# Kernel tuning notes

Measured on AMD Instinct MI355X. Metric: run time of the kernel, lower is better.

The kernel has to match this reference:

```python
import jax, jax.numpy as jnp
import numpy as np

N = 8192
D_IN = 512
D_HID = 256
D_OUT = 128
NEG_SLOPE = 0.25
MASK_VAL = -1.0e12
EDGE_PROB = 0.004  # avg degree ~33


def _leaky(x):
    return jax.nn.leaky_relu(x, NEG_SLOPE)


def setup_inputs() -> dict:
    key = jax.random.key(0)
    ks = jax.random.split(key, 9)
    x = jax.random.normal(ks[0], (N, D_IN), jnp.float32)
    # sparse-ish normalized adjacency, stored dense (torch uses sparse mm / to_dense)
    vals = jax.random.uniform(ks[1], (N, N), jnp.float32)
    mask = jax.random.uniform(ks[2], (N, N)) < EDGE_PROB
    adj = jnp.where(mask, vals, 0.0).astype(jnp.float32)
    W1 = jax.random.normal(ks[3], (D_IN, D_HID), jnp.float32) * (2.0 / (D_IN + D_HID)) ** 0.5
    b1 = jnp.zeros((D_HID,), jnp.float32)
    W2 = jax.random.normal(ks[4], (D_HID, D_HID), jnp.float32) * (1.0 / D_HID) ** 0.5
    b2 = jnp.zeros((D_HID,), jnp.float32)
    Wg = jax.random.normal(ks[5], (D_HID, D_OUT), jnp.float32) * (2.0 / (D_HID + D_OUT)) ** 0.5
    a = jax.random.normal(ks[6], (2 * D_OUT, 1), jnp.float32) * 0.1
    return dict(x=x, adj=adj, W1=W1, b1=b1, W2=W2, b2=b2, Wg=Wg, a=a)


def reference(x, adj, W1, b1, W2, b2, Wg, a):
    # GCN layer 1: adj @ (x @ W1) + b1, leaky_relu (dropout p=0 / eval -> identity)
    x1 = _leaky(adj @ (x @ W1) + b1)
    # GCN layer 2
    x2 = _leaky(adj @ (x1 @ W2) + b2)
    # GAT layer: h = x2 @ Wg; e[i,j] = leaky_relu([h_i || h_j] @ a)
    # identical to leaky_relu((h@a1)_i + (h@a2)_j) without the O(N^2*2F) concat
    h = x2 @ Wg                              # [N, D_OUT]
    a1 = a[:D_OUT, 0]
    a2 = a[D_OUT:, 0]
    e = _leaky((h @ a1)[:, None] + (h @ a2)[None, :])  # [N, N]
    att = jnp.where(adj > 0, e, MASK_VAL)
    att = jax.nn.softmax(att, axis=1)
    h_prime = att @ h                        # [N, D_OUT] (concat=False -> no elu)
    out = _leaky(h_prime)
    mu = out[:, : D_OUT // 2]
    logvar = out[:, D_OUT // 2 :]
    return mu, logvar
```

## Files before the change

### kernel.cpp

```cpp
#include <hip/hip_runtime.h>

typedef unsigned short u16;
typedef u16 u16x4 __attribute__((ext_vector_type(4)));
typedef __bf16 bf16x8 __attribute__((ext_vector_type(8)));
typedef float f32x4 __attribute__((ext_vector_type(4)));

#define NROW 8192
#define CAP 128
#define D_IN 512
#define D_HID 256
#define D_OUT 128

__device__ __forceinline__ float leaky_f(float x) { return x > 0.f ? x : 0.25f * x; }

__device__ __forceinline__ u16 f2bf_rne(float f) {
  unsigned u = __float_as_uint(f);
  u += 0x7fffu + ((u >> 16) & 1u);
  return (u16)(u >> 16);
}
__device__ __forceinline__ void split_bf16(float f, u16& hi, u16& lo) {
  hi = f2bf_rne(f);
  float fh = __uint_as_float(((unsigned)hi) << 16);
  lo = f2bf_rne(f - fh);
}

__global__ __launch_bounds__(256) void k_csr_packw(const float* __restrict__ adj,
    int* __restrict__ cnt, int* __restrict__ cols, float* __restrict__ vals,
    const float* __restrict__ W1, u16* __restrict__ B1,
    const float* __restrict__ W2, u16* __restrict__ B2,
    const float* __restrict__ Wg, u16* __restrict__ B3) {
  int b = blockIdx.x;
  if (b < NROW) {
    int i = b;
    __shared__ int c;
    if (threadIdx.x == 0) c = 0;
    __syncthreads();
    const float4* row = (const float4*)(adj + (size_t)i * NROW);
    for (int j4 = threadIdx.x; j4 < NROW / 4; j4 += 256) {
      float4 v = row[j4];
      int base = j4 * 4;
      if (v.x > 0.f) { int s = atomicAdd(&c, 1); if (s < CAP) { cols[i*CAP+s] = base;   vals[i*CAP+s] = v.x; } }
      if (v.y > 0.f) { int s = atomicAdd(&c, 1); if (s < CAP) { cols[i*CAP+s] = base+1; vals[i*CAP+s] = v.y; } }
      if (v.z > 0.f) { int s = atomicAdd(&c, 1); if (s < CAP) { cols[i*CAP+s] = base+2; vals[i*CAP+s] = v.z; } }
      if (v.w > 0.f) { int s = atomicAdd(&c, 1); if (s < CAP) { cols[i*CAP+s] = base+3; vals[i*CAP+s] = v.w; } }
    }
    __syncthreads();
    if (threadIdx.x == 0) cnt[i] = (c < CAP) ? c : CAP;
    return;
  }
  const float* W; u16* Bt; int K, Nc, id;
  int pb = b - NROW;
  if (pb < 512)      { W = W1; Bt = B1; K = D_IN;  Nc = D_HID; id = pb * 256 + threadIdx.x; }
  else if (pb < 768) { W = W2; Bt = B2; K = D_HID; Nc = D_HID; id = (pb - 512) * 256 + threadIdx.x; }
  else               { W = Wg; Bt = B3; K = D_HID; Nc = D_OUT; id = (pb - 768) * 256 + threadIdx.x; }
  int n = id % Nc, k = id / Nc;
  float f = W[id];
  u16 hi, lo; split_bf16(f, hi, lo);
  size_t ro = (size_t)n * 2 * K;
  Bt[ro + k] = hi; Bt[ro + K + k] = lo;
}

__global__ __launch_bounds__(256) void k_gemm_x(const float* __restrict__ X, const u16* __restrict__ Bt,
    float* __restrict__ C, int N, int K) {
  __shared__ u16 Ah[64 * 40], Al[64 * 40];
  __shared__ u16 Bh[64 * 40], Bl[64 * 40];
  int tid = threadIdx.x;
  int bm = blockIdx.y * 64, bn = blockIdx.x * 64;
  int wave = tid >> 6, lane = tid & 63, l15 = lane & 15, quad = lane >> 4;
  f32x4 acc[4] = {};
  int ar = tid >> 2, aj = (tid & 3) << 3;
  const float* Xrow = X + (size_t)(bm + ar) * K + aj;
  const u16* Brow = Bt + (size_t)(bn + ar) * (2 * K) + aj;
  for (int k0 = 0; k0 < K; k0 += 32) {
    alignas(16) u16 hh[8], ll[8];
    float xv[8];
    *(float4*)(xv)     = *(const float4*)(Xrow + k0);
    *(float4*)(xv + 4) = *(const float4*)(Xrow + k0 + 4);
#pragma unroll
    for (int e = 0; e < 8; ++e) split_bf16(xv[e], hh[e], ll[e]);
    *(uint4*)(&Ah[ar * 40 + aj]) = *(const uint4*)hh;
    *(uint4*)(&Al[ar * 40 + aj]) = *(const uint4*)ll;
    *(uint4*)(&Bh[ar * 40 + aj]) = *(const uint4*)(Brow + k0);
    *(uint4*)(&Bl[ar * 40 + aj]) = *(const uint4*)(Brow + K + k0);
    __syncthreads();
    bf16x8 afh = *(const bf16x8*)(&Ah[(wave * 16 + l15) * 40 + quad * 8]);
    bf16x8 afl = *(const bf16x8*)(&Al[(wave * 16 + l15) * 40 + quad * 8]);
#pragma unroll
    for (int c = 0; c < 4; ++c) {
      bf16x8 bfh = *(const bf16x8*)(&Bh[(c * 16 + l15) * 40 + quad * 8]);
      bf16x8 bfl = *(const bf16x8*)(&Bl[(c * 16 + l15) * 40 + quad * 8]);
      acc[c] = __builtin_amdgcn_mfma_f32_16x16x32_bf16(afh, bfh, acc[c], 0, 0, 0);
      acc[c] = __builtin_amdgcn_mfma_f32_16x16x32_bf16(afh, bfl, acc[c], 0, 0, 0);
      acc[c] = __builtin_amdgcn_mfma_f32_16x16x32_bf16(afl, bfh, acc[c], 0, 0, 0);
    }
    __syncthreads();
  }
#pragma unroll
  for (int c = 0; c < 4; ++c)
#pragma unroll
    for (int rg = 0; rg < 4; ++rg) {
      int rowi = bm + wave * 16 + quad * 4 + rg;
      int coli = bn + c * 16 + l15;
      C[(size_t)rowi * N + coli] = acc[c][rg];
    }
}

__global__ __launch_bounds__(256) void k_gemm(const u16* __restrict__ A, const u16* __restrict__ Bt,
    float* __restrict__ C, int N, int K) {
  __shared__ u16 Ah[64 * 40], Al[64 * 40];
  __shared__ u16 Bh[64 * 40], Bl[64 * 40];
  int tid = threadIdx.x;
  int bm = blockIdx.y * 64, bn = blockIdx.x * 64;
  int wave = tid >> 6, lane = tid & 63, l15 = lane & 15, quad = lane >> 4;
  f32x4 acc[4] = {};
  int ar = tid >> 2, aj = (tid & 3) << 3;
  const u16* Arow = A + (size_t)(bm + ar) * (2 * K) + aj;
  const u16* Brow = Bt + (size_t)(bn + ar) * (2 * K) + aj;
  for (int k0 = 0; k0 < K; k0 += 32) {
    *(uint4*)(&Ah[ar * 40 + aj]) = *(const uint4*)(Arow + k0);
    *(uint4*)(&Al[ar * 40 + aj]) = *(const uint4*)(Arow + K + k0);
    *(uint4*)(&Bh[ar * 40 + aj]) = *(const uint4*)(Brow + k0);
    *(uint4*)(&Bl[ar * 40 + aj]) = *(const uint4*)(Brow + K + k0);
    __syncthreads();
    bf16x8 afh = *(const bf16x8*)(&Ah[(wave * 16 + l15) * 40 + quad * 8]);
    bf16x8 afl = *(const bf16x8*)(&Al[(wave * 16 + l15) * 40 + quad * 8]);
#pragma unroll
    for (int c = 0; c < 4; ++c) {
      bf16x8 bfh = *(const bf16x8*)(&Bh[(c * 16 + l15) * 40 + quad * 8]);
      bf16x8 bfl = *(const bf16x8*)(&Bl[(c * 16 + l15) * 40 + quad * 8]);
      acc[c] = __builtin_amdgcn_mfma_f32_16x16x32_bf16(afh, bfh, acc[c], 0, 0, 0);
      acc[c] = __builtin_amdgcn_mfma_f32_16x16x32_bf16(afh, bfl, acc[c], 0, 0, 0);
      acc[c] = __builtin_amdgcn_mfma_f32_16x16x32_bf16(afl, bfh, acc[c], 0, 0, 0);
    }
    __syncthreads();
  }
#pragma unroll
  for (int c = 0; c < 4; ++c)
#pragma unroll
    for (int rg = 0; rg < 4; ++rg) {
      int rowi = bm + wave * 16 + quad * 4 + rg;
      int coli = bn + c * 16 + l15;
      C[(size_t)rowi * N + coli] = acc[c][rg];
    }
}

__global__ __launch_bounds__(256) void k_gemm3(const u16* __restrict__ A, const u16* __restrict__ Bt,
    float* __restrict__ C, int K,
    const float* __restrict__ aptr, float* __restrict__ s1, float* __restrict__ s2) {
  __shared__ u16 Ah[32 * 40], Al[32 * 40];
  __shared__ u16 Bh[128 * 40], Bl[128 * 40];
  __shared__ float sp1[2][32], sp2[2][32];
  int tid = threadIdx.x;
  int bm = blockIdx.y * 32;
  int wave = tid >> 6, lane = tid & 63, l15 = lane & 15, quad = lane >> 4;
  int rhalf = wave >> 1, chalf = wave & 1;
  f32x4 acc[4] = {};
  int t7 = tid & 127;
  int ar = t7 >> 2, aj = (t7 & 3) << 3;
  int br = tid >> 1, bj = (tid & 1) << 4;
  const u16* Arow = A + (size_t)(bm + ar) * (2 * K) + aj + (tid < 128 ? 0 : K);
  u16* Adst = (tid < 128 ? Ah : Al) + ar * 40 + aj;
  const u16* Brow = Bt + (size_t)br * (2 * K) + bj;
  for (int k0 = 0; k0 < K; k0 += 32) {
    *(uint4*)Adst = *(const uint4*)(Arow + k0);
#pragma unroll
    for (int jj = 0; jj < 2; ++jj) {
      *(uint4*)(&Bh[br * 40 + bj + jj * 8]) = *(const uint4*)(Brow + k0 + jj * 8);
      *(uint4*)(&Bl[br * 40 + bj + jj * 8]) = *(const uint4*)(Brow + K + k0 + jj * 8);
    }
    __syncthreads();
    bf16x8 afh = *(const bf16x8*)(&Ah[(rhalf * 16 + l15) * 40 + quad * 8]);
    bf16x8 afl = *(const bf16x8*)(&Al[(rhalf * 16 + l15) * 40 + quad * 8]);
#pragma unroll
    for (int c = 0; c < 4; ++c) {
      bf16x8 bfh = *(const bf16x8*)(&Bh[(chalf * 64 + c * 16 + l15) * 40 + quad * 8]);
      bf16x8 bfl = *(const bf16x8*)(&Bl[(chalf * 64 + c * 16 + l15) * 40 + quad * 8]);
      acc[c] = __builtin_amdgcn_mfma_f32_16x16x32_bf16(afh, bfh, acc[c], 0, 0, 0);
      acc[c] = __builtin_amdgcn_mfma_f32_16x16x32_bf16(afh, bfl, acc[c], 0, 0, 0);
      acc[c] = __builtin_amdgcn_mfma_f32_16x16x32_bf16(afl, bfh, acc[c], 0, 0, 0);
    }
    __syncthreads();
  }
#pragma unroll
  for (int c = 0; c < 4; ++c)
#pragma unroll
    for (int rg = 0; rg < 4; ++rg) {
      int rowi = bm + rhalf * 16 + quad * 4 + rg;
      int coli = chalf * 64 + c * 16 + l15;
      C[(size_t)rowi * 128 + coli] = acc[c][rg];
    }
  float a1v[4], a2v[4];
#pragma unroll
  for (int c = 0; c < 4; ++c) {
    a1v[c] = aptr[chalf * 64 + c * 16 + l15];
    a2v[c] = aptr[128 + chalf * 64 + c * 16 + l15];
  }
#pragma unroll
  for (int rg = 0; rg < 4; ++rg) {
    float p1 = 0.f, p2 = 0.f;
#pragma unroll
    for (int c = 0; c < 4; ++c) { p1 = fmaf(acc[c][rg], a1v[c], p1); p2 = fmaf(acc[c][rg], a2v[c], p2); }
#pragma unroll
    for (int m = 1; m < 16; m <<= 1) { p1 += __shfl_xor(p1, m); p2 += __shfl_xor(p2, m); }
    if (l15 == 0) {
      int rloc = rhalf * 16 + quad * 4 + rg;
      sp1[chalf][rloc] = p1; sp2[chalf][rloc] = p2;
    }
  }
  __syncthreads();
  if (tid < 32) {
    s1[bm + tid] = sp1[0][tid] + sp1[1][tid];
    s2[bm + tid] = sp2[0][tid] + sp2[1][tid];
  }
}

__global__ __launch_bounds__(256) void k_spmm_pack(const float* __restrict__ Hin,
    const float* __restrict__ bias, const int* __restrict__ cnt,
    const int* __restrict__ cols, const float* __restrict__ vals, u16* __restrict__ Ap) {
  int i = blockIdx.x, t = threadIdx.x;
  int t64 = t & 63, g = t >> 6;
  __shared__ int sc[CAP];
  __shared__ float sv[CAP];
  __shared__ float4 sacc[4][64];
  int n = cnt[i];
  if (t < n) { sc[t] = cols[i * CAP + t]; sv[t] = vals[i * CAP + t]; }
  __syncthreads();
  float4 acc = {0.f, 0.f, 0.f, 0.f};
  const float4* H4 = (const float4*)Hin;
  for (int k = g; k < n; k += 4) {
    float w = sv[k];
    float4 v = H4[(size_t)sc[k] * 64 + t64];
    acc.x = fmaf(w, v.x, acc.x); acc.y = fmaf(w, v.y, acc.y);
    acc.z = fmaf(w, v.z, acc.z); acc.w = fmaf(w, v.w, acc.w);
  }
  sacc[g][t64] = acc;
  __syncthreads();
  if (t < 64) {
    float4 a0 = sacc[0][t], a1 = sacc[1][t], a2 = sacc[2][t], a3 = sacc[3][t];
    float4 bv = ((const float4*)bias)[t];
    float r[4] = { leaky_f(a0.x + a1.x + a2.x + a3.x + bv.x),
                   leaky_f(a0.y + a1.y + a2.y + a3.y + bv.y),
                   leaky_f(a0.z + a1.z + a2.z + a3.z + bv.z),
                   leaky_f(a0.w + a1.w + a2.w + a3.w + bv.w) };
    u16x4 hi4, lo4;
#pragma unroll
    for (int e = 0; e < 4; ++e) { u16 hh, ll; split_bf16(r[e], hh, ll); hi4[e] = hh; lo4[e] = ll; }
    size_t ro = (size_t)i * 512;
    *(u16x4*)(Ap + ro + 4 * t) = hi4;
    *(u16x4*)(Ap + ro + 256 + 4 * t) = lo4;
  }
}

__global__ __launch_bounds__(128) void k_attn(const float* __restrict__ h,
    const float* __restrict__ s1, const float* __restrict__ s2,
    const int* __restrict__ cnt, const int* __restrict__ cols, float* __restrict__ out) {
  int i = blockIdx.x, t = threadIdx.x;
  int t32 = t & 31, g = t >> 5;
  __shared__ int sc[CAP];
  __shared__ float sw[CAP];
  __shared__ float sred[2];
  __shared__ float4 sacc[4][32];
  int n = cnt[i];
  float s1i = s1[i];
  if (t < n) { int c = cols[i * CAP + t]; sc[t] = c; sw[t] = leaky_f(s1i + s2[c]); }
  __syncthreads();
  if (t < 64) {
    float m = -1e30f;
    if (t < n) m = sw[t];
    if (t + 64 < n) m = fmaxf(m, sw[t + 64]);
    for (int o = 32; o > 0; o >>= 1) m = fmaxf(m, __shfl_down(m, o));
    if (t == 0) sred[0] = m;
  }
  __syncthreads();
  float mx = sred[0];
  if (t < n) sw[t] = expf(sw[t] - mx);
  __syncthreads();
  if (t < 64) {
    float s = 0.f;
    if (t < n) s = sw[t];
    if (t + 64 < n) s += sw[t + 64];
    for (int o = 32; o > 0; o >>= 1) s += __shfl_down(s, o);
    if (t == 0) sred[1] = s;
  }
  __syncthreads();
  float inv = (n > 0) ? 1.0f / sred[1] : 0.f;
  float4 acc = {0.f, 0.f, 0.f, 0.f};
  const float4* h4 = (const float4*)h;
  for (int k = g; k < n; k += 4) {
    float w = sw[k];
    float4 v = h4[(size_t)sc[k] * 32 + t32];
    acc.x = fmaf(w, v.x, acc.x); acc.y = fmaf(w, v.y, acc.y);
    acc.z = fmaf(w, v.z, acc.z); acc.w = fmaf(w, v.w, acc.w);
  }
  sacc[g][t32] = acc;
  __syncthreads();
  if (t < 32) {
    float4 a0 = sacc[0][t], a1 = sacc[1][t], a2 = sacc[2][t], a3 = sacc[3][t];
    float4 r;
    r.x = leaky_f((a0.x + a1.x + a2.x + a3.x) * inv);
    r.y = leaky_f((a0.y + a1.y + a2.y + a3.y) * inv);
    r.z = leaky_f((a0.z + a1.z + a2.z + a3.z) * inv);
    r.w = leaky_f((a0.w + a1.w + a2.w + a3.w) * inv);
    float4* o4 = (float4*)out;
    if (t < 16) o4[(size_t)i * 16 + t] = r;
    else        o4[(size_t)NROW * 16 + (size_t)i * 16 + (t - 16)] = r;
  }
}

extern "C" void kernel_launch(void* const* d_in, const int* in_sizes, int n_in,
                              void* d_out, int out_size, void* d_ws, size_t ws_size,
                              hipStream_t stream) {
  const float* x   = (const float*)d_in[0];
  const float* adj = (const float*)d_in[1];
  const float* W1  = (const float*)d_in[2];
  const float* b1  = (const float*)d_in[3];
  const float* W2  = (const float*)d_in[4];
  const float* b2  = (const float*)d_in[5];
  const float* Wg  = (const float*)d_in[6];
  const float* a   = (const float*)d_in[7];
  float* out = (float*)d_out;

  char* ws = (char*)d_ws;
  int*   row_cnt  = (int*)  (ws + 0);
  int*   row_cols = (int*)  (ws + 32768);
  float* row_vals = (float*)(ws + 4227072);
  u16*   B1t      = (u16*)  (ws + 8421376);
  u16*   B2t      = (u16*)  (ws + 8945664);
  u16*   B3t      = (u16*)  (ws + 9207808);
  float* s1       = (float*)(ws + 9338880);
  float* s2       = (float*)(ws + 9371648);
  float* h        = (float*)(ws + 9404416);
  float* H0T2     = (float*)(ws + 13598720);
  u16*   Apack    = (u16*)  (ws + 21987328);

  k_csr_packw<<<NROW + 896, 256, 0, stream>>>(adj, row_cnt, row_cols, row_vals,
                                              W1, B1t, W2, B2t, Wg, B3t);
  k_gemm_x<<<dim3(4, 128), 256, 0, stream>>>(x, B1t, H0T2, D_HID, D_IN);
  k_spmm_pack<<<NROW, 256, 0, stream>>>(H0T2, b1, row_cnt, row_cols, row_vals, Apack);
  k_gemm<<<dim3(4, 128), 256, 0, stream>>>(Apack, B2t, H0T2, D_HID, D_HID);
  k_spmm_pack<<<NROW, 256, 0, stream>>>(H0T2, b2, row_cnt, row_cols, row_vals, Apack);
  k_gemm3<<<dim3(1, 256), 256, 0, stream>>>(Apack, B3t, h, D_HID, a, s1, s2);
  k_attn<<<NROW, 128, 0, stream>>>(h, s1, s2, row_cnt, row_cols, out);
}
```

Measured before the change: 494.4 us.

## Fuse CSR build with first GEMM and store GAT features as bf16

Moves the CSR extraction of the dense adjacency out of the weight-packing kernel and into the first x@W1 GEMM launch, so the memory-bound adjacency scan runs alongside the MFMA GEMM blocks. Weight packing now runs as its own small kernel first. Separately, the GAT feature matrix h is written as bf16 instead of fp32, halving the bytes gathered in the attention aggregation. The bf16 storage of h lowers precision of the final output.

```diff
diff --git a/kernel.cpp b/kernel.cpp
--- a/kernel.cpp
+++ b/kernel.cpp
@@ -18,38 +18,19 @@
   u += 0x7fffu + ((u >> 16) & 1u);
   return (u16)(u >> 16);
 }
+__device__ __forceinline__ float bf2f(u16 v) { return __uint_as_float(((unsigned)v) << 16); }
 __device__ __forceinline__ void split_bf16(float f, u16& hi, u16& lo) {
   hi = f2bf_rne(f);
   float fh = __uint_as_float(((unsigned)hi) << 16);
   lo = f2bf_rne(f - fh);
 }
 
-__global__ __launch_bounds__(256) void k_csr_packw(const float* __restrict__ adj,
-    int* __restrict__ cnt, int* __restrict__ cols, float* __restrict__ vals,
+__global__ __launch_bounds__(256) void k_packw(
     const float* __restrict__ W1, u16* __restrict__ B1,
     const float* __restrict__ W2, u16* __restrict__ B2,
     const float* __restrict__ Wg, u16* __restrict__ B3) {
-  int b = blockIdx.x;
-  if (b < NROW) {
-    int i = b;
-    __shared__ int c;
-    if (threadIdx.x == 0) c = 0;
-    __syncthreads();
-    const float4* row = (const float4*)(adj + (size_t)i * NROW);
-    for (int j4 = threadIdx.x; j4 < NROW / 4; j4 += 256) {
-      float4 v = row[j4];
-      int base = j4 * 4;
-      if (v.x > 0.f) { int s = atomicAdd(&c, 1); if (s < CAP) { cols[i*CAP+s] = base;   vals[i*CAP+s] = v.x; } }
-      if (v.y > 0.f) { int s = atomicAdd(&c, 1); if (s < CAP) { cols[i*CAP+s] = base+1; vals[i*CAP+s] = v.y; } }
-      if (v.z > 0.f) { int s = atomicAdd(&c, 1); if (s < CAP) { cols[i*CAP+s] = base+2; vals[i*CAP+s] = v.z; } }
-      if (v.w > 0.f) { int s = atomicAdd(&c, 1); if (s < CAP) { cols[i*CAP+s] = base+3; vals[i*CAP+s] = v.w; } }
-    }
-    __syncthreads();
-    if (threadIdx.x == 0) cnt[i] = (c < CAP) ? c : CAP;
-    return;
-  }
   const float* W; u16* Bt; int K, Nc, id;
-  int pb = b - NROW;
+  int pb = blockIdx.x;
   if (pb < 512)      { W = W1; Bt = B1; K = D_IN;  Nc = D_HID; id = pb * 256 + threadIdx.x; }
   else if (pb < 768) { W = W2; Bt = B2; K = D_HID; Nc = D_HID; id = (pb - 512) * 256 + threadIdx.x; }
   else               { W = Wg; Bt = B3; K = D_HID; Nc = D_OUT; id = (pb - 768) * 256 + threadIdx.x; }
@@ -60,49 +41,70 @@
   Bt[ro + k] = hi; Bt[ro + K + k] = lo;
 }
 
-__global__ __launch_bounds__(256) void k_gemm_x(const float* __restrict__ X, const u16* __restrict__ Bt,
-    float* __restrict__ C, int N, int K) {
+__global__ __launch_bounds__(256) void k_csr_gemm1(const float* __restrict__ adj,
+    int* __restrict__ cnt, int* __restrict__ cols, float* __restrict__ vals,
+    const float* __restrict__ X, const u16* __restrict__ Bt, float* __restrict__ C) {
   __shared__ u16 Ah[64 * 40], Al[64 * 40];
   __shared__ u16 Bh[64 * 40], Bl[64 * 40];
+  __shared__ int csrc;
+  int b = blockIdx.x;
   int tid = threadIdx.x;
-  int bm = blockIdx.y * 64, bn = blockIdx.x * 64;
-  int wave = tid >> 6, lane = tid & 63, l15 = lane & 15, quad = lane >> 4;
-  f32x4 acc[4] = {};
-  int ar = tid >> 2, aj = (tid & 3) << 3;
-  const float* Xrow = X + (size_t)(bm + ar) * K + aj;
-  const u16* Brow = Bt + (size_t)(bn + ar) * (2 * K) + aj;
-  for (int k0 = 0; k0 < K; k0 += 32) {
-    alignas(16) u16 hh[8], ll[8];
-    float xv[8];
-    *(float4*)(xv)     = *(const float4*)(Xrow + k0);
-    *(float4*)(xv + 4) = *(const float4*)(Xrow + k0 + 4);
-#pragma unroll
-    for (int e = 0; e < 8; ++e) split_bf16(xv[e], hh[e], ll[e]);
-    *(uint4*)(&Ah[ar * 40 + aj]) = *(const uint4*)hh;
-    *(uint4*)(&Al[ar * 40 + aj]) = *(const uint4*)ll;
-    *(uint4*)(&Bh[ar * 40 + aj]) = *(const uint4*)(Brow + k0);
-    *(uint4*)(&Bl[ar * 40 + aj]) = *(const uint4*)(Brow + K + k0);
-    __syncthreads();
-    bf16x8 afh = *(const bf16x8*)(&Ah[(wave * 16 + l15) * 40 + quad * 8]);
-    bf16x8 afl = *(const bf16x8*)(&Al[(wave * 16 + l15) * 40 + quad * 8]);
-#pragma unroll
-    for (int c = 0; c < 4; ++c) {
-      bf16x8 bfh = *(const bf16x8*)(&Bh[(c * 16 + l15) * 40 + quad * 8]);
-      bf16x8 bfl = *(const bf16x8*)(&Bl[(c * 16 + l15) * 40 + quad * 8]);
-      acc[c] = __builtin_amdgcn_mfma_f32_16x16x32_bf16(afh, bfh, acc[c], 0, 0, 0);
-      acc[c] = __builtin_amdgcn_mfma_f32_16x16x32_bf16(afh, bfl, acc[c], 0, 0, 0);
-      acc[c] = __builtin_amdgcn_mfma_f32_16x16x32_bf16(afl, bfh, acc[c], 0, 0, 0);
-    }
-    __syncthreads();
-  }
-#pragma unroll
-  for (int c = 0; c < 4; ++c)
-#pragma unroll
-    for (int rg = 0; rg < 4; ++rg) {
-      int rowi = bm + wave * 16 + quad * 4 + rg;
-      int coli = bn + c * 16 + l15;
-      C[(size_t)rowi * N + coli] = acc[c][rg];
-    }
+  if (b < 512) {
+    const int N = D_HID, K = D_IN;
+    int bm = (b >> 2) * 64, bn = (b & 3) * 64;
+    int wave = tid >> 6, lane = tid & 63, l15 = lane & 15, quad = lane >> 4;
+    f32x4 acc[4] = {};
+    int ar = tid >> 2, aj = (tid & 3) << 3;
+    const float* Xrow = X + (size_t)(bm + ar) * K + aj;
+    const u16* Brow = Bt + (size_t)(bn + ar) * (2 * K) + aj;
+    for (int k0 = 0; k0 < K; k0 += 32) {
+      alignas(16) u16 hh[8], ll[8];
+      float xv[8];
+      *(float4*)(xv)     = *(const float4*)(Xrow + k0);
+      *(float4*)(xv + 4) = *(const float4*)(Xrow + k0 + 4);
+#pragma unroll
+      for (int e = 0; e < 8; ++e) split_bf16(xv[e], hh[e], ll[e]);
+      *(uint4*)(&Ah[ar * 40 + aj]) = *(const uint4*)hh;
+      *(uint4*)(&Al[ar * 40 + aj]) = *(const uint4*)ll;
+      *(uint4*)(&Bh[ar * 40 + aj]) = *(const uint4*)(Brow + k0);
+      *(uint4*)(&Bl[ar * 40 + aj]) = *(const uint4*)(Brow + K + k0);
+      __syncthreads();
+      bf16x8 afh = *(const bf16x8*)(&Ah[(wave * 16 + l15) * 40 + quad * 8]);
+      bf16x8 afl = *(const bf16x8*)(&Al[(wave * 16 + l15) * 40 + quad * 8]);
+#pragma unroll
+      for (int c = 0; c < 4; ++c) {
+        bf16x8 bfh = *(const bf16x8*)(&Bh[(c * 16 + l15) * 40 + quad * 8]);
+        bf16x8 bfl = *(const bf16x8*)(&Bl[(c * 16 + l15) * 40 + quad * 8]);
+        acc[c] = __builtin_amdgcn_mfma_f32_16x16x32_bf16(afh, bfh, acc[c], 0, 0, 0);
+        acc[c] = __builtin_amdgcn_mfma_f32_16x16x32_bf16(afh, bfl, acc[c], 0, 0, 0);
+        acc[c] = __builtin_amdgcn_mfma_f32_16x16x32_bf16(afl, bfh, acc[c], 0, 0, 0);
+      }
+      __syncthreads();
+    }
+#pragma unroll
+    for (int c = 0; c < 4; ++c)
+#pragma unroll
+      for (int rg = 0; rg < 4; ++rg) {
+        int rowi = bm + wave * 16 + quad * 4 + rg;
+        int coli = bn + c * 16 + l15;
+        C[(size_t)rowi * N + coli] = acc[c][rg];
+      }
+    return;
+  }
+  int i = b - 512;
+  if (tid == 0) csrc = 0;
+  __syncthreads();
+  const float4* row = (const float4*)(adj + (size_t)i * NROW);
+  for (int j4 = tid; j4 < NROW / 4; j4 += 256) {
+    float4 v = row[j4];
+    int base = j4 * 4;
+    if (v.x > 0.f) { int s = atomicAdd(&csrc, 1); if (s < CAP) { cols[i*CAP+s] = base;   vals[i*CAP+s] = v.x; } }
+    if (v.y > 0.f) { int s = atomicAdd(&csrc, 1); if (s < CAP) { cols[i*CAP+s] = base+1; vals[i*CAP+s] = v.y; } }
+    if (v.z > 0.f) { int s = atomicAdd(&csrc, 1); if (s < CAP) { cols[i*CAP+s] = base+2; vals[i*CAP+s] = v.z; } }
+    if (v.w > 0.f) { int s = atomicAdd(&csrc, 1); if (s < CAP) { cols[i*CAP+s] = base+3; vals[i*CAP+s] = v.w; } }
+  }
+  __syncthreads();
+  if (tid == 0) cnt[i] = (csrc < CAP) ? csrc : CAP;
 }
 
 __global__ __launch_bounds__(256) void k_gemm(const u16* __restrict__ A, const u16* __restrict__ Bt,
@@ -145,7 +147,7 @@
 }
 
 __global__ __launch_bounds__(256) void k_gemm3(const u16* __restrict__ A, const u16* __restrict__ Bt,
-    float* __restrict__ C, int K,
+    u16* __restrict__ Hb, int K,
     const float* __restrict__ aptr, float* __restrict__ s1, float* __restrict__ s2) {
   __shared__ u16 Ah[32 * 40], Al[32 * 40];
   __shared__ u16 Bh[128 * 40], Bl[128 * 40];
@@ -187,7 +189,7 @@
     for (int rg = 0; rg < 4; ++rg) {
       int rowi = bm + rhalf * 16 + quad * 4 + rg;
       int coli = chalf * 64 + c * 16 + l15;
-      C[(size_t)rowi * 128 + coli] = acc[c][rg];
+      Hb[(size_t)rowi * 128 + coli] = f2bf_rne(acc[c][rg]);
     }
   float a1v[4], a2v[4];
 #pragma unroll
@@ -251,7 +253,7 @@
   }
 }
 
-__global__ __launch_bounds__(128) void k_attn(const float* __restrict__ h,
+__global__ __launch_bounds__(128) void k_attn(const u16* __restrict__ Hb,
     const float* __restrict__ s1, const float* __restrict__ s2,
     const int* __restrict__ cnt, const int* __restrict__ cols, float* __restrict__ out) {
   int i = blockIdx.x, t = threadIdx.x;
@@ -285,12 +287,11 @@
   __syncthreads();
   float inv = (n > 0) ? 1.0f / sred[1] : 0.f;
   float4 acc = {0.f, 0.f, 0.f, 0.f};
-  const float4* h4 = (const float4*)h;
   for (int k = g; k < n; k += 4) {
     float w = sw[k];
-    float4 v = h4[(size_t)sc[k] * 32 + t32];
-    acc.x = fmaf(w, v.x, acc.x); acc.y = fmaf(w, v.y, acc.y);
-    acc.z = fmaf(w, v.z, acc.z); acc.w = fmaf(w, v.w, acc.w);
+    u16x4 v = *(const u16x4*)(Hb + (size_t)sc[k] * 128 + 4 * t32);
+    acc.x = fmaf(w, bf2f(v[0]), acc.x); acc.y = fmaf(w, bf2f(v[1]), acc.y);
+    acc.z = fmaf(w, bf2f(v[2]), acc.z); acc.w = fmaf(w, bf2f(v[3]), acc.w);
   }
   sacc[g][t32] = acc;
   __syncthreads();
@@ -329,16 +330,15 @@
   u16*   B3t      = (u16*)  (ws + 9207808);
   float* s1       = (float*)(ws + 9338880);
   float* s2       = (float*)(ws + 9371648);
-  float* h        = (float*)(ws + 9404416);
+  u16*   hbf      = (u16*)  (ws + 9404416);
   float* H0T2     = (float*)(ws + 13598720);
   u16*   Apack    = (u16*)  (ws + 21987328);
 
-  k_csr_packw<<<NROW + 896, 256, 0, stream>>>(adj, row_cnt, row_cols, row_vals,
-                                              W1, B1t, W2, B2t, Wg, B3t);
-  k_gemm_x<<<dim3(4, 128), 256, 0, stream>>>(x, B1t, H0T2, D_HID, D_IN);
+  k_packw<<<896, 256, 0, stream>>>(W1, B1t, W2, B2t, Wg, B3t);
+  k_csr_gemm1<<<512 + NROW, 256, 0, stream>>>(adj, row_cnt, row_cols, row_vals, x, B1t, H0T2);
   k_spmm_pack<<<NROW, 256, 0, stream>>>(H0T2, b1, row_cnt, row_cols, row_vals, Apack);
   k_gemm<<<dim3(4, 128), 256, 0, stream>>>(Apack, B2t, H0T2, D_HID, D_HID);
   k_spmm_pack<<<NROW, 256, 0, stream>>>(H0T2, b2, row_cnt, row_cols, row_vals, Apack);
-  k_gemm3<<<dim3(1, 256), 256, 0, stream>>>(Apack, B3t, h, D_HID, a, s1, s2);
-  k_attn<<<NROW, 128, 0, stream>>>(h, s1, s2, row_cnt, row_cols, out);
-}
+  k_gemm3<<<dim3(1, 256), 256, 0, stream>>>(Apack, B3t, hbf, D_HID, a, s1, s2);
+  k_attn<<<NROW, 128, 0, stream>>>(hbf, s1, s2, row_cnt, row_cols, out);
+}
```

After: 471.9 us. 1.05x faster.
